# Kernel optimization log

Measured on AMD Instinct MI355X. Metric: run time of the kernel, lower is better.

The kernel has to match this reference:

```python
import jax, jax.numpy as jnp
import numpy as np

N_DIRS = 16384
D_MODEL = 1024
BATCH = 4096
K = 32
MULTIK = 128  # min(4*K, N_DIRS)
AUXK = 256
DEAD_STEPS_THRESHOLD = 266


def setup_inputs() -> dict:
    key = jax.random.key(0)
    k1, k2, k3, k4, k5, k6 = jax.random.split(key, 6)
    return {
        "x": jax.random.normal(k1, (BATCH, D_MODEL), dtype=jnp.float32),
        "W_enc": jax.random.normal(k2, (N_DIRS, D_MODEL), dtype=jnp.float32) * 0.02,
        "W_dec": jax.random.normal(k3, (D_MODEL, N_DIRS), dtype=jnp.float32) * 0.02,
        "pre_bias": jax.random.normal(k4, (D_MODEL,), dtype=jnp.float32) * 0.02,
        "latent_bias": jax.random.normal(k5, (N_DIRS,), dtype=jnp.float32) * 0.02,
        "stats_last_nonzero": jax.random.randint(k6, (N_DIRS,), 0, 512, dtype=jnp.int64)
        if jax.config.jax_enable_x64 else
        jax.random.randint(k6, (N_DIRS,), 0, 512, dtype=jnp.int32),
    }


def _scatter_topk(pre, k):
    """top-k on last dim, relu values, scatter into dense zeros (k-sparse SAE)."""
    vals, idx = jax.lax.top_k(pre, k)          # [B, k]
    vals = jax.nn.relu(vals)
    rows = jnp.arange(pre.shape[0])[:, None]   # [B, 1]
    dense = jnp.zeros_like(pre).at[rows, idx].set(vals)
    return vals, idx, dense


def reference(x, W_enc, W_dec, pre_bias, latent_bias, stats_last_nonzero):
    xc = x - pre_bias                                   # [B, d_model]
    latents_pre_act = xc @ W_enc.T + latent_bias        # [B, n_dirs]

    topk_values, topk_indices, latents = _scatter_topk(latents_pre_act, K)
    multik_values, multik_indices, multik_latents = _scatter_topk(latents_pre_act, MULTIK)

    recons = latents @ W_dec.T + pre_bias               # [B, d_model]
    multik_recons = multik_latents @ W_dec.T + pre_bias

    # auxk on dead latents (stats buffer is a constant snapshot here)
    dead_mask = (stats_last_nonzero > DEAD_STEPS_THRESHOLD).astype(latents_pre_act.dtype)
    auxk_values, auxk_indices = jax.lax.top_k(latents_pre_act * dead_mask, AUXK)
    auxk_values = jax.nn.relu(auxk_values)

    return (recons, multik_recons, topk_values, topk_indices,
            auxk_values, auxk_indices, latents_pre_act, latents)
```

## Files before the change

kernel.cpp:

```cpp
#include <hip/hip_runtime.h>
#include <hip/hip_bf16.h>
#include <cstdint>

#define NDIRS 16384
#define DMODEL 1024
#define BATCH 4096
#define KTOP 32
#define MKK 128
#define AUXK 256
#define DEADTHR 266
#define CAND_MAX 2048
#define FOLD_T0 31

__device__ __forceinline__ unsigned fkey(float f) {
  unsigned u = __float_as_uint(f);
  return (u & 0x80000000u) ? ~u : (u | 0x80000000u);
}

__global__ __launch_bounds__(256) void k_transpose(const float* __restrict__ Wdec,
                                                   float* __restrict__ WdT) {
  __shared__ float tile[32][33];
  const int tx = threadIdx.x & 31, ty = threadIdx.x >> 5;
  const int c0 = blockIdx.x * 32;
  const int r0 = blockIdx.y * 32;
#pragma unroll
  for (int i = 0; i < 32; i += 8)
    tile[ty + i][tx] = Wdec[(size_t)(r0 + ty + i) * NDIRS + c0 + tx];
  __syncthreads();
#pragma unroll
  for (int i = 0; i < 32; i += 8)
    WdT[(size_t)(c0 + ty + i) * DMODEL + r0 + tx] = tile[tx][ty + i];
}

__global__ __launch_bounds__(256, 2) void k_gemm_enc(
    const float* __restrict__ x, const float* __restrict__ Wenc,
    const float* __restrict__ pre_bias, const float* __restrict__ lat_bias,
    float* __restrict__ P) {
  __shared__ __align__(16) float As[2][16][132];
  __shared__ __align__(16) float Bs[2][16][132];
  const int t = threadIdx.x;
  const int tx = t & 15, ty = t >> 4;
  const int bn = blockIdx.x;
  const int bm = blockIdx.y;
  const int lr = t >> 2;
  const int lk = (t & 3) << 2;

  const float* xA = x + (size_t)(bm * 128 + lr) * DMODEL;
  const float* wB = Wenc + (size_t)(bn * 128 + lr) * DMODEL;

  float acc[8][8];
#pragma unroll
  for (int i = 0; i < 8; ++i)
#pragma unroll
    for (int j = 0; j < 8; ++j) acc[i][j] = 0.f;

  const int c0 = bn * 128 + tx * 8;
  const int rdA = ty * 8;
  const int rdB = tx * 8;

  float4 pb = *(const float4*)(pre_bias + lk);
  float4 a0 = *(const float4*)(xA + lk);
  float4 a1 = *(const float4*)(xA + (size_t)64 * DMODEL + lk);
  float4 b0 = *(const float4*)(wB + lk);
  float4 b1 = *(const float4*)(wB + (size_t)64 * DMODEL + lk);

  int cur = 0;
  for (int tt = 0; tt < DMODEL / 16; ++tt) {
    As[cur][lk + 0][lr] = a0.x - pb.x;
    As[cur][lk + 1][lr] = a0.y - pb.y;
    As[cur][lk + 2][lr] = a0.z - pb.z;
    As[cur][lk + 3][lr] = a0.w - pb.w;
    As[cur][lk + 0][lr + 64] = a1.x - pb.x;
    As[cur][lk + 1][lr + 64] = a1.y - pb.y;
    As[cur][lk + 2][lr + 64] = a1.z - pb.z;
    As[cur][lk + 3][lr + 64] = a1.w - pb.w;
    Bs[cur][lk + 0][lr] = b0.x;  Bs[cur][lk + 1][lr] = b0.y;
    Bs[cur][lk + 2][lr] = b0.z;  Bs[cur][lk + 3][lr] = b0.w;
    Bs[cur][lk + 0][lr + 64] = b1.x;  Bs[cur][lk + 1][lr + 64] = b1.y;
    Bs[cur][lk + 2][lr + 64] = b1.z;  Bs[cur][lk + 3][lr + 64] = b1.w;
    __syncthreads();
    if (tt < DMODEL / 16 - 1) {
      const int k0 = (tt + 1) * 16;
      pb = *(const float4*)(pre_bias + k0 + lk);
      a0 = *(const float4*)(xA + k0 + lk);
      a1 = *(const float4*)(xA + (size_t)64 * DMODEL + k0 + lk);
      b0 = *(const float4*)(wB + k0 + lk);
      b1 = *(const float4*)(wB + (size_t)64 * DMODEL + k0 + lk);
    }
#pragma unroll
    for (int k = 0; k < 16; ++k) {
      float a[8], b[8];
      *(float4*)&a[0] = *(const float4*)&As[cur][k][rdA];
      *(float4*)&a[4] = *(const float4*)&As[cur][k][rdA + 4];
      *(float4*)&b[0] = *(const float4*)&Bs[cur][k][rdB];
      *(float4*)&b[4] = *(const float4*)&Bs[cur][k][rdB + 4];
#pragma unroll
      for (int i = 0; i < 8; ++i)
#pragma unroll
        for (int j = 0; j < 8; ++j) acc[i][j] = fmaf(a[i], b[j], acc[i][j]);
    }
    if (tt == FOLD_T0) {
#pragma unroll
      for (int i = 0; i < 8; ++i) {
        const size_t ro = (size_t)(bm * 128 + ty * 8 + i) * NDIRS + c0;
        *(float4*)(P + ro) = *(float4*)&acc[i][0];
        *(float4*)(P + ro + 4) = *(float4*)&acc[i][4];
#pragma unroll
        for (int j = 0; j < 8; ++j) acc[i][j] = 0.f;
      }
    }
    cur ^= 1;
  }

  float lb8[8];
  *(float4*)&lb8[0] = *(const float4*)(lat_bias + c0);
  *(float4*)&lb8[4] = *(const float4*)(lat_bias + c0 + 4);
#pragma unroll
  for (int i = 0; i < 8; ++i) {
    const size_t ro = (size_t)(bm * 128 + ty * 8 + i) * NDIRS + c0;
    float p0[8];
    *(float4*)&p0[0] = *(const float4*)(P + ro);
    *(float4*)&p0[4] = *(const float4*)(P + ro + 4);
    float o[8];
#pragma unroll
    for (int j = 0; j < 8; ++j) o[j] = (p0[j] + acc[i][j]) + lb8[j];
    *(float4*)(P + ro) = *(float4*)&o[0];
    *(float4*)(P + ro + 4) = *(float4*)&o[4];
  }
}

__global__ __launch_bounds__(256) void k_select(
    const float* __restrict__ P, const int* __restrict__ stats,
    float* __restrict__ topk_v, float* __restrict__ topk_i,
    float* __restrict__ auxk_v, float* __restrict__ auxk_i,
    float* __restrict__ latents, float* __restrict__ mval,
    int* __restrict__ midx) {
  __shared__ unsigned histA[2048];
  __shared__ unsigned histD[2048];
  __shared__ unsigned chunk[256];
  __shared__ __align__(16) unsigned char uni[32768];
  __shared__ float sTopV[KTOP];
  __shared__ int sTopI[KTOP];
  __shared__ unsigned cntA, cntD, sTa, sTd;

  unsigned (*pkA)[1024] = (unsigned(*)[1024])uni;
  unsigned (*pkD)[1024] = (unsigned(*)[1024])(uni + 16384);
  unsigned* candKeyA = (unsigned*)uni;
  unsigned short* candIdxA = (unsigned short*)(uni + 8192);
  unsigned* candKeyD = (unsigned*)(uni + 12288);
  unsigned short* candIdxD = (unsigned short*)(uni + 20480);

  const int t = threadIdx.x;
  const int w = t >> 6;
  const int b = blockIdx.x;
  const float* rp = P + (size_t)b * NDIRS;

  for (int i = t; i < 8192; i += 256) ((unsigned*)uni)[i] = 0;
  if (t == 0) { cntA = 0; cntD = 0; sTa = 0; sTd = 0; }
  __syncthreads();
#pragma unroll
  for (int i = 0; i < 16; ++i) {
    const int e = (i * 256 + t) * 4;
    const float4 v = *(const float4*)(rp + e);
    const int4 s = *(const int4*)(stats + e);
    const float hv[4] = {v.x, v.y, v.z, v.w};
    const int sv[4] = {s.x, s.y, s.z, s.w};
#pragma unroll
    for (int c = 0; c < 4; ++c) {
      const unsigned bin = fkey(hv[c]) >> 21;
      const unsigned inc = 1u << ((bin & 1) << 4);
      atomicAdd(&pkA[w][bin >> 1], inc);
      if (sv[c] > DEADTHR && hv[c] > 0.f) atomicAdd(&pkD[w][bin >> 1], inc);
    }
  }
  __syncthreads();
  for (int i = t; i < 2048; i += 256) {
    const int word = i >> 1, sh = (i & 1) << 4;
    unsigned sa = 0, sd = 0;
#pragma unroll
    for (int q = 0; q < 4; ++q) {
      sa += (pkA[q][word] >> sh) & 0xFFFFu;
      sd += (pkD[q][word] >> sh) & 0xFFFFu;
    }
    histA[i] = sa;
    histD[i] = sd;
  }
  __syncthreads();
  {
    unsigned cs = 0;
#pragma unroll
    for (int j = 0; j < 8; ++j) cs += histA[t * 8 + j];
    chunk[t] = cs;
    __syncthreads();
    for (int s = 1; s < 256; s <<= 1) {
      unsigned add = (t + s < 256) ? chunk[t + s] : 0;
      __syncthreads();
      chunk[t] += add;
      __syncthreads();
    }
    unsigned suf = (t + 1 < 256) ? chunk[t + 1] : 0;
    for (int j = 7; j >= 0; --j) {
      const unsigned h = histA[t * 8 + j];
      const unsigned ab = suf;
      suf += h;
      if (suf >= MKK && ab < MKK) sTa = (unsigned)(t * 8 + j);
    }
  }
  __syncthreads();
  {
    unsigned cs = 0;
#pragma unroll
    for (int j = 0; j < 8; ++j) cs += histD[t * 8 + j];
    chunk[t] = cs;
    __syncthreads();
    for (int s = 1; s < 256; s <<= 1) {
      unsigned add = (t + s < 256) ? chunk[t + s] : 0;
      __syncthreads();
      chunk[t] += add;
      __syncthreads();
    }
    unsigned suf = (t + 1 < 256) ? chunk[t + 1] : 0;
    for (int j = 7; j >= 0; --j) {
      const unsigned h = histD[t * 8 + j];
      const unsigned ab = suf;
      suf += h;
      if (suf >= AUXK && ab < AUXK) sTd = (unsigned)(t * 8 + j);
    }
  }
  __syncthreads();
  {
    const unsigned Ta = sTa, Td = sTd;
#pragma unroll
    for (int i = 0; i < 16; ++i) {
      const int e = (i * 256 + t) * 4;
      const float4 v = *(const float4*)(rp + e);
      const int4 s = *(const int4*)(stats + e);
      const float hv[4] = {v.x, v.y, v.z, v.w};
      const int sv[4] = {s.x, s.y, s.z, s.w};
#pragma unroll
      for (int c = 0; c < 4; ++c) {
        const unsigned k = fkey(hv[c]);
        const unsigned bin = k >> 21;
        if (bin >= Ta) {
          unsigned p = atomicAdd(&cntA, 1u);
          if (p < CAND_MAX) { candKeyA[p] = k; candIdxA[p] = (unsigned short)(e + c); }
        }
        if (sv[c] > DEADTHR && hv[c] > 0.f && bin >= Td) {
          unsigned p = atomicAdd(&cntD, 1u);
          if (p < CAND_MAX) { candKeyD[p] = k; candIdxD[p] = (unsigned short)(e + c); }
        }
      }
    }
  }
  __syncthreads();
  {
    const unsigned C = cntA < CAND_MAX ? cntA : CAND_MAX;
    for (unsigned i = t; i < C; i += 256) {
      const unsigned ki = candKeyA[i];
      const unsigned ii = candIdxA[i];
      unsigned r = 0;
      for (unsigned j = 0; j < C; ++j) {
        const unsigned kj = candKeyA[j];
        r += (unsigned)((kj > ki) | ((kj == ki) & (candIdxA[j] < ii)));
      }
      if (r < MKK) {
        const float vr = fmaxf(rp[ii], 0.f);
        mval[b * MKK + r] = vr;
        midx[b * MKK + r] = (int)ii;
        if (r < KTOP) {
          topk_v[b * KTOP + r] = vr;
          topk_i[b * KTOP + r] = (float)ii;
          sTopV[r] = vr;
          sTopI[r] = (int)ii;
        }
      }
    }
  }
  {
    const unsigned C = cntD < CAND_MAX ? cntD : CAND_MAX;
    for (unsigned i = t; i < C; i += 256) {
      const unsigned ki = candKeyD[i];
      const unsigned ii = candIdxD[i];
      unsigned r = 0;
      for (unsigned j = 0; j < C; ++j) {
        const unsigned kj = candKeyD[j];
        r += (unsigned)((kj > ki) | ((kj == ki) & (candIdxD[j] < ii)));
      }
      if (r < AUXK) {
        auxk_v[b * AUXK + r] = fmaxf(rp[ii], 0.f);
        auxk_i[b * AUXK + r] = (float)ii;
      }
    }
    if (t == 0 && C < AUXK) {
      for (unsigned r = C; r < AUXK; ++r) {
        auxk_v[b * AUXK + r] = 0.f;
        auxk_i[b * AUXK + r] = 0.f;
      }
    }
  }
  __syncthreads();
  float* latRow = latents + (size_t)b * NDIRS;
  const float4 z4 = make_float4(0.f, 0.f, 0.f, 0.f);
#pragma unroll
  for (int i = 0; i < 16; ++i) *(float4*)(latRow + (i * 256 + t) * 4) = z4;
  __syncthreads();
  if (t < KTOP) latRow[sTopI[t]] = sTopV[t];
}

__global__ __launch_bounds__(256) void k_recons(
    const float* __restrict__ WdT, const float* __restrict__ mval,
    const int* __restrict__ midx, const float* __restrict__ pre_bias,
    float* __restrict__ recons, float* __restrict__ mrecons) {
  __shared__ float sv[MKK];
  __shared__ int si[MKK];
  const int t = threadIdx.x;
  const int b = blockIdx.x;
  if (t < MKK) {
    sv[t] = mval[b * MKK + t];
    si[t] = midx[b * MKK + t];
  }
  __syncthreads();
  const int d = t * 4;
  float4 acc = *(const float4*)(pre_bias + d);
#pragma unroll 4
  for (int i = 0; i < KTOP; ++i) {
    const float v = sv[i];
    const float4 wv = *(const float4*)(WdT + (size_t)si[i] * DMODEL + d);
    acc.x = fmaf(v, wv.x, acc.x);
    acc.y = fmaf(v, wv.y, acc.y);
    acc.z = fmaf(v, wv.z, acc.z);
    acc.w = fmaf(v, wv.w, acc.w);
  }
  *(float4*)(recons + (size_t)b * DMODEL + d) = acc;
#pragma unroll 4
  for (int i = KTOP; i < MKK; ++i) {
    const float v = sv[i];
    const float4 wv = *(const float4*)(WdT + (size_t)si[i] * DMODEL + d);
    acc.x = fmaf(v, wv.x, acc.x);
    acc.y = fmaf(v, wv.y, acc.y);
    acc.z = fmaf(v, wv.z, acc.z);
    acc.w = fmaf(v, wv.w, acc.w);
  }
  *(float4*)(mrecons + (size_t)b * DMODEL + d) = acc;
}

__global__ __launch_bounds__(256) void k_recons_g(
    const float* __restrict__ Wdec, const float* __restrict__ mval,
    const int* __restrict__ midx, const float* __restrict__ pre_bias,
    float* __restrict__ recons, float* __restrict__ mrecons) {
  __shared__ float sv[MKK];
  __shared__ int si[MKK];
  const int t = threadIdx.x;
  const int b = blockIdx.x;
  if (t < MKK) {
    sv[t] = mval[b * MKK + t];
    si[t] = midx[b * MKK + t];
  }
  __syncthreads();
  const int d = t * 4;
  float4 acc = *(const float4*)(pre_bias + d);
#pragma unroll 2
  for (int i = 0; i < MKK; ++i) {
    const float v = sv[i];
    const int j = si[i];
    acc.x = fmaf(v, Wdec[(size_t)(d + 0) * NDIRS + j], acc.x);
    acc.y = fmaf(v, Wdec[(size_t)(d + 1) * NDIRS + j], acc.y);
    acc.z = fmaf(v, Wdec[(size_t)(d + 2) * NDIRS + j], acc.z);
    acc.w = fmaf(v, Wdec[(size_t)(d + 3) * NDIRS + j], acc.w);
    if (i == KTOP - 1) *(float4*)(recons + (size_t)b * DMODEL + d) = acc;
  }
  *(float4*)(mrecons + (size_t)b * DMODEL + d) = acc;
}

extern "C" void kernel_launch(void* const* d_in, const int* in_sizes, int n_in,
                              void* d_out, int out_size, void* d_ws,
                              size_t ws_size, hipStream_t stream) {
  const float* x = (const float*)d_in[0];
  const float* Wenc = (const float*)d_in[1];
  const float* Wdec = (const float*)d_in[2];
  const float* pre_bias = (const float*)d_in[3];
  const float* lat_bias = (const float*)d_in[4];
  const int* stats = (const int*)d_in[5];

  float* out = (float*)d_out;
  float* recons = out;
  float* mrecons = recons + (size_t)BATCH * DMODEL;
  float* topk_v = mrecons + (size_t)BATCH * DMODEL;
  float* topk_i = topk_v + (size_t)BATCH * KTOP;
  float* auxk_v = topk_i + (size_t)BATCH * KTOP;
  float* auxk_i = auxk_v + (size_t)BATCH * AUXK;
  float* P = auxk_i + (size_t)BATCH * AUXK;
  float* latents = P + (size_t)BATCH * NDIRS;

  const size_t mval_b = (size_t)BATCH * MKK * sizeof(float);
  const size_t wdT_b = (size_t)NDIRS * DMODEL * sizeof(float);

  float* mval = (float*)d_ws;
  int* midx = (int*)((char*)mval + mval_b);
  float* WdT = (float*)((char*)midx + mval_b);
  const bool useT = ws_size >= 2 * mval_b + wdT_b;

  if (useT) {
    dim3 g(NDIRS / 32, DMODEL / 32);
    k_transpose<<<g, 256, 0, stream>>>(Wdec, WdT);
  }
  {
    dim3 g(NDIRS / 128, BATCH / 128);
    k_gemm_enc<<<g, 256, 0, stream>>>(x, Wenc, pre_bias, lat_bias, P);
  }
  k_select<<<BATCH, 256, 0, stream>>>(P, stats, topk_v, topk_i, auxk_v, auxk_i,
                                      latents, mval, midx);
  if (useT)
    k_recons<<<BATCH, 256, 0, stream>>>(WdT, mval, midx, pre_bias, recons, mrecons);
  else
    k_recons_g<<<BATCH, 256, 0, stream>>>(Wdec, mval, midx, pre_bias, recons, mrecons);
}
```

Before: 2.359 ms.

## Fuse select and reconstruction kernels; keep split-K partial in registers

The top-k selection kernel now performs the decoder reconstruction directly from shared-memory top-128 values and indices. This removes the separate recons kernel and the workspace round-trip for mval/midx. The encoder GEMM also keeps its first partial sum in a second register array instead of writing it to P and reading it back. That avoids a full extra pass over the 256 MB pre-activation matrix, but it doubles the accumulator registers, which risks spills or lower occupancy under launch_bounds(256,2).

```diff
diff --git a/kernel.cpp b/kernel.cpp
--- a/kernel.cpp
+++ b/kernel.cpp
@@ -49,10 +49,11 @@
   const float* wB = Wenc + (size_t)(bn * 128 + lr) * DMODEL;
 
   float acc[8][8];
+  float tot[8][8];
 #pragma unroll
   for (int i = 0; i < 8; ++i)
 #pragma unroll
-    for (int j = 0; j < 8; ++j) acc[i][j] = 0.f;
+    for (int j = 0; j < 8; ++j) { acc[i][j] = 0.f; tot[i][j] = 0.f; }
 
   const int c0 = bn * 128 + tx * 8;
   const int rdA = ty * 8;
@@ -101,13 +102,9 @@
     }
     if (tt == FOLD_T0) {
 #pragma unroll
-      for (int i = 0; i < 8; ++i) {
-        const size_t ro = (size_t)(bm * 128 + ty * 8 + i) * NDIRS + c0;
-        *(float4*)(P + ro) = *(float4*)&acc[i][0];
-        *(float4*)(P + ro + 4) = *(float4*)&acc[i][4];
-#pragma unroll
-        for (int j = 0; j < 8; ++j) acc[i][j] = 0.f;
-      }
+      for (int i = 0; i < 8; ++i)
+#pragma unroll
+        for (int j = 0; j < 8; ++j) { tot[i][j] = acc[i][j]; acc[i][j] = 0.f; }
     }
     cur ^= 1;
   }
@@ -118,29 +115,29 @@
 #pragma unroll
   for (int i = 0; i < 8; ++i) {
     const size_t ro = (size_t)(bm * 128 + ty * 8 + i) * NDIRS + c0;
-    float p0[8];
-    *(float4*)&p0[0] = *(const float4*)(P + ro);
-    *(float4*)&p0[4] = *(const float4*)(P + ro + 4);
     float o[8];
 #pragma unroll
-    for (int j = 0; j < 8; ++j) o[j] = (p0[j] + acc[i][j]) + lb8[j];
+    for (int j = 0; j < 8; ++j) o[j] = (tot[i][j] + acc[i][j]) + lb8[j];
     *(float4*)(P + ro) = *(float4*)&o[0];
     *(float4*)(P + ro + 4) = *(float4*)&o[4];
   }
 }
 
-__global__ __launch_bounds__(256) void k_select(
+template <bool USET>
+__global__ __launch_bounds__(256) void k_select_recons(
     const float* __restrict__ P, const int* __restrict__ stats,
+    const float* __restrict__ Wd,
+    const float* __restrict__ pre_bias,
     float* __restrict__ topk_v, float* __restrict__ topk_i,
     float* __restrict__ auxk_v, float* __restrict__ auxk_i,
-    float* __restrict__ latents, float* __restrict__ mval,
-    int* __restrict__ midx) {
+    float* __restrict__ latents, float* __restrict__ recons,
+    float* __restrict__ mrecons) {
   __shared__ unsigned histA[2048];
   __shared__ unsigned histD[2048];
   __shared__ unsigned chunk[256];
   __shared__ __align__(16) unsigned char uni[32768];
-  __shared__ float sTopV[KTOP];
-  __shared__ int sTopI[KTOP];
+  __shared__ float sv[MKK];
+  __shared__ int si[MKK];
   __shared__ unsigned cntA, cntD, sTa, sTd;
 
   unsigned (*pkA)[1024] = (unsigned(*)[1024])uni;
@@ -164,13 +161,13 @@
     const float4 v = *(const float4*)(rp + e);
     const int4 s = *(const int4*)(stats + e);
     const float hv[4] = {v.x, v.y, v.z, v.w};
-    const int sv[4] = {s.x, s.y, s.z, s.w};
+    const int sx[4] = {s.x, s.y, s.z, s.w};
 #pragma unroll
     for (int c = 0; c < 4; ++c) {
       const unsigned bin = fkey(hv[c]) >> 21;
       const unsigned inc = 1u << ((bin & 1) << 4);
       atomicAdd(&pkA[w][bin >> 1], inc);
-      if (sv[c] > DEADTHR && hv[c] > 0.f) atomicAdd(&pkD[w][bin >> 1], inc);
+      if (sx[c] > DEADTHR && hv[c] > 0.f) atomicAdd(&pkD[w][bin >> 1], inc);
     }
   }
   __syncthreads();
@@ -236,7 +233,7 @@
       const float4 v = *(const float4*)(rp + e);
       const int4 s = *(const int4*)(stats + e);
       const float hv[4] = {v.x, v.y, v.z, v.w};
-      const int sv[4] = {s.x, s.y, s.z, s.w};
+      const int sx[4] = {s.x, s.y, s.z, s.w};
 #pragma unroll
       for (int c = 0; c < 4; ++c) {
         const unsigned k = fkey(hv[c]);
@@ -245,7 +242,7 @@
           unsigned p = atomicAdd(&cntA, 1u);
           if (p < CAND_MAX) { candKeyA[p] = k; candIdxA[p] = (unsigned short)(e + c); }
         }
-        if (sv[c] > DEADTHR && hv[c] > 0.f && bin >= Td) {
+        if (sx[c] > DEADTHR && hv[c] > 0.f && bin >= Td) {
           unsigned p = atomicAdd(&cntD, 1u);
           if (p < CAND_MAX) { candKeyD[p] = k; candIdxD[p] = (unsigned short)(e + c); }
         }
@@ -265,13 +262,11 @@
       }
       if (r < MKK) {
         const float vr = fmaxf(rp[ii], 0.f);
-        mval[b * MKK + r] = vr;
-        midx[b * MKK + r] = (int)ii;
+        sv[r] = vr;
+        si[r] = (int)ii;
         if (r < KTOP) {
           topk_v[b * KTOP + r] = vr;
           topk_i[b * KTOP + r] = (float)ii;
-          sTopV[r] = vr;
-          sTopI[r] = (int)ii;
         }
       }
     }
@@ -303,73 +298,43 @@
   const float4 z4 = make_float4(0.f, 0.f, 0.f, 0.f);
 #pragma unroll
   for (int i = 0; i < 16; ++i) *(float4*)(latRow + (i * 256 + t) * 4) = z4;
-  __syncthreads();
-  if (t < KTOP) latRow[sTopI[t]] = sTopV[t];
-}
-
-__global__ __launch_bounds__(256) void k_recons(
-    const float* __restrict__ WdT, const float* __restrict__ mval,
-    const int* __restrict__ midx, const float* __restrict__ pre_bias,
-    float* __restrict__ recons, float* __restrict__ mrecons) {
-  __shared__ float sv[MKK];
-  __shared__ int si[MKK];
-  const int t = threadIdx.x;
-  const int b = blockIdx.x;
-  if (t < MKK) {
-    sv[t] = mval[b * MKK + t];
-    si[t] = midx[b * MKK + t];
-  }
-  __syncthreads();
+  if (t < KTOP) latRow[si[t]] = sv[t];
   const int d = t * 4;
   float4 acc = *(const float4*)(pre_bias + d);
+  if (USET) {
 #pragma unroll 4
-  for (int i = 0; i < KTOP; ++i) {
-    const float v = sv[i];
-    const float4 wv = *(const float4*)(WdT + (size_t)si[i] * DMODEL + d);
-    acc.x = fmaf(v, wv.x, acc.x);
-    acc.y = fmaf(v, wv.y, acc.y);
-    acc.z = fmaf(v, wv.z, acc.z);
-    acc.w = fmaf(v, wv.w, acc.w);
-  }
-  *(float4*)(recons + (size_t)b * DMODEL + d) = acc;
+    for (int i = 0; i < KTOP; ++i) {
+      const float v = sv[i];
+      const float4 wv = *(const float4*)(Wd + (size_t)si[i] * DMODEL + d);
+      acc.x = fmaf(v, wv.x, acc.x);
+      acc.y = fmaf(v, wv.y, acc.y);
+      acc.z = fmaf(v, wv.z, acc.z);
+      acc.w = fmaf(v, wv.w, acc.w);
+    }
+    *(float4*)(recons + (size_t)b * DMODEL + d) = acc;
 #pragma unroll 4
-  for (int i = KTOP; i < MKK; ++i) {
-    const float v = sv[i];
-    const float4 wv = *(const float4*)(WdT + (size_t)si[i] * DMODEL + d);
-    acc.x = fmaf(v, wv.x, acc.x);
-    acc.y = fmaf(v, wv.y, acc.y);
-    acc.z = fmaf(v, wv.z, acc.z);
-    acc.w = fmaf(v, wv.w, acc.w);
-  }
-  *(float4*)(mrecons + (size_t)b * DMODEL + d) = acc;
-}
-
-__global__ __launch_bounds__(256) void k_recons_g(
-    const float* __restrict__ Wdec, const float* __restrict__ mval,
-    const int* __restrict__ midx, const float* __restrict__ pre_bias,
-    float* __restrict__ recons, float* __restrict__ mrecons) {
-  __shared__ float sv[MKK];
-  __shared__ int si[MKK];
-  const int t = threadIdx.x;
-  const int b = blockIdx.x;
-  if (t < MKK) {
-    sv[t] = mval[b * MKK + t];
-    si[t] = midx[b * MKK + t];
-  }
-  __syncthreads();
-  const int d = t * 4;
-  float4 acc = *(const float4*)(pre_bias + d);
+    for (int i = KTOP; i < MKK; ++i) {
+      const float v = sv[i];
+      const float4 wv = *(const float4*)(Wd + (size_t)si[i] * DMODEL + d);
+      acc.x = fmaf(v, wv.x, acc.x);
+      acc.y = fmaf(v, wv.y, acc.y);
+      acc.z = fmaf(v, wv.z, acc.z);
+      acc.w = fmaf(v, wv.w, acc.w);
+    }
+    *(float4*)(mrecons + (size_t)b * DMODEL + d) = acc;
+  } else {
 #pragma unroll 2
-  for (int i = 0; i < MKK; ++i) {
-    const float v = sv[i];
-    const int j = si[i];
-    acc.x = fmaf(v, Wdec[(size_t)(d + 0) * NDIRS + j], acc.x);
-    acc.y = fmaf(v, Wdec[(size_t)(d + 1) * NDIRS + j], acc.y);
-    acc.z = fmaf(v, Wdec[(size_t)(d + 2) * NDIRS + j], acc.z);
-    acc.w = fmaf(v, Wdec[(size_t)(d + 3) * NDIRS + j], acc.w);
-    if (i == KTOP - 1) *(float4*)(recons + (size_t)b * DMODEL + d) = acc;
-  }
-  *(float4*)(mrecons + (size_t)b * DMODEL + d) = acc;
+    for (int i = 0; i < MKK; ++i) {
+      const float v = sv[i];
+      const int j = si[i];
+      acc.x = fmaf(v, Wd[(size_t)(d + 0) * NDIRS + j], acc.x);
+      acc.y = fmaf(v, Wd[(size_t)(d + 1) * NDIRS + j], acc.y);
+      acc.z = fmaf(v, Wd[(size_t)(d + 2) * NDIRS + j], acc.z);
+      acc.w = fmaf(v, Wd[(size_t)(d + 3) * NDIRS + j], acc.w);
+      if (i == KTOP - 1) *(float4*)(recons + (size_t)b * DMODEL + d) = acc;
+    }
+    *(float4*)(mrecons + (size_t)b * DMODEL + d) = acc;
+  }
 }
 
 extern "C" void kernel_launch(void* const* d_in, const int* in_sizes, int n_in,
@@ -392,13 +357,9 @@
   float* P = auxk_i + (size_t)BATCH * AUXK;
   float* latents = P + (size_t)BATCH * NDIRS;
 
-  const size_t mval_b = (size_t)BATCH * MKK * sizeof(float);
   const size_t wdT_b = (size_t)NDIRS * DMODEL * sizeof(float);
-
-  float* mval = (float*)d_ws;
-  int* midx = (int*)((char*)mval + mval_b);
-  float* WdT = (float*)((char*)midx + mval_b);
-  const bool useT = ws_size >= 2 * mval_b + wdT_b;
+  float* WdT = (float*)d_ws;
+  const bool useT = ws_size >= wdT_b;
 
   if (useT) {
     dim3 g(NDIRS / 32, DMODEL / 32);
@@ -408,10 +369,12 @@
     dim3 g(NDIRS / 128, BATCH / 128);
     k_gemm_enc<<<g, 256, 0, stream>>>(x, Wenc, pre_bias, lat_bias, P);
   }
-  k_select<<<BATCH, 256, 0, stream>>>(P, stats, topk_v, topk_i, auxk_v, auxk_i,
-                                      latents, mval, midx);
   if (useT)
-    k_recons<<<BATCH, 256, 0, stream>>>(WdT, mval, midx, pre_bias, recons, mrecons);
+    k_select_recons<true><<<BATCH, 256, 0, stream>>>(
+        P, stats, WdT, pre_bias, topk_v, topk_i, auxk_v, auxk_i, latents,
+        recons, mrecons);
   else
-    k_recons_g<<<BATCH, 256, 0, stream>>>(Wdec, mval, midx, pre_bias, recons, mrecons);
-}
+    k_select_recons<false><<<BATCH, 256, 0, stream>>>(
+        P, stats, Wdec, pre_bias, topk_v, topk_i, auxk_v, auxk_i, latents,
+        recons, mrecons);
+}
```

Measured after the change: 2.316 ms. About the same (-1.8%).
